# Kernel optimization log

Hardware: AMD Instinct MI355X
Metric: run time of the kernel (lower is better)

Reference implementation:

```python
import jax, jax.numpy as jnp
import numpy as np

B, S, E, H = 2, 2048, 1024, 16
Dh = E // H  # 64
KEEP = 0.9   # 1 - dropout_p
INV_SCALE = 1.0  # forward() default; call site does not pass inv_scale


def setup_inputs() -> dict:
    key = jax.random.key(0)
    ks = jax.random.split(key, 12)
    query = jax.random.normal(ks[0], (B, S, E), dtype=jnp.float32)
    key_t = jax.random.normal(ks[1], (B, S, E), dtype=jnp.float32)
    value = jax.random.normal(ks[2], (B, S, E), dtype=jnp.float32)
    attn_mask = jax.random.randint(ks[3], (B, S), 0, 2, dtype=jnp.int32)
    # pre-scaled inverted dropout keep-mask (deterministic stand-in for F.dropout)
    dropout_mask = (jax.random.uniform(ks[4], (B, H, S, S)) < KEEP).astype(jnp.float32) / KEEP
    Wq = jax.random.normal(ks[5], (E, E), dtype=jnp.float32) * 0.02
    bq = jnp.zeros((E,), dtype=jnp.float32)
    Wk = jax.random.normal(ks[6], (E, E), dtype=jnp.float32) * 0.02
    bk = jnp.zeros((E,), dtype=jnp.float32)
    Wv = jax.random.normal(ks[7], (E, E), dtype=jnp.float32) * 0.02
    bv = jnp.zeros((E,), dtype=jnp.float32)
    return {"query": query, "key": key_t, "value": value, "attn_mask": attn_mask,
            "dropout_mask": dropout_mask, "Wq": Wq, "bq": bq, "Wk": Wk, "bk": bk,
            "Wv": Wv, "bv": bv}


def _heads(x, W, b):
    # Linear then split heads: (B,S,E) -> (B,H,S,Dh)
    y = x @ W.T + b
    return y.reshape(B, S, H, Dh).transpose(0, 2, 1, 3)


def reference(query, key, value, attn_mask, dropout_mask, Wq, bq, Wk, bk, Wv, bv):
    q = _heads(query, Wq, bq)
    k = _heads(key, Wk, bk)
    v = _heads(value, Wv, bv)
    scores = jnp.einsum("bhqd,bhkd->bhqk", q, k) / INV_SCALE
    pad = (attn_mask == 0)[:, None, None, :]  # (B,1,1,S) True = masked
    scores = jnp.where(pad, -jnp.inf, scores)
    attn = jax.nn.softmax(scores, axis=-1) * dropout_mask
    out = jnp.einsum("bhqk,bhkd->bhqd", attn, v)  # (B,H,S,Dh)
    return out
```

## Files before the change

kernel.cpp:

```cpp
#include <hip/hip_runtime.h>

#define B_ 2
#define S_ 2048
#define E_ 1024
#define H_ 16
#define DH 64
#define MM (B_*S_)
#define BHN (B_*H_)
#define KSPLIT 4

typedef unsigned short u16;
typedef unsigned int u32;
typedef __attribute__((ext_vector_type(8))) __bf16 bf16x8;
typedef __attribute__((ext_vector_type(8))) _Float16 f16x8;
typedef __attribute__((ext_vector_type(4))) float f32x4;
typedef __attribute__((ext_vector_type(8))) u16 u16x8;
typedef __attribute__((ext_vector_type(4))) u16 u16x4;

static __device__ __forceinline__ u16 f2bf(float f) {
  u32 u = __builtin_bit_cast(u32, f);
  u += 0x7fffu + ((u >> 16) & 1u);
  return (u16)(u >> 16);
}
static __device__ __forceinline__ float bf2f(u16 h) {
  return __builtin_bit_cast(float, (u32)h << 16);
}
static __device__ __forceinline__ u32 sw(u32 byte) {
  return byte ^ (((byte >> 7) & 7u) << 4);
}
static __device__ __forceinline__ bf16x8 frag(const u16* lds, u32 byte) {
  return *(const bf16x8*)((const char*)lds + byte);
}
static __device__ __forceinline__ f16x8 frag16(const u16* lds, u32 byte) {
  return *(const f16x8*)((const char*)lds + byte);
}
static __device__ __forceinline__ f32x4 mfma_bf(bf16x8 a, bf16x8 b, f32x4 c) {
  return __builtin_amdgcn_mfma_f32_16x16x32_bf16(a, b, c, 0, 0, 0);
}
static __device__ __forceinline__ f32x4 mfma_f16(f16x8 a, f16x8 b, f32x4 c) {
  return __builtin_amdgcn_mfma_f32_16x16x32_f16(a, b, c, 0, 0, 0);
}
static __device__ __forceinline__ void gload_lds16(const u16* g, u16* lds_base) {
  __builtin_amdgcn_global_load_lds(
      (const __attribute__((address_space(1))) u32*)g,
      (__attribute__((address_space(3))) u32*)lds_base, 16, 0, 0);
}

#define L2E 1.44269504088896340736f

struct SplitArg { const float* s; u16* h; u16* l; int n4; };

__global__ void split6_kernel(SplitArg a0, SplitArg a1, SplitArg a2,
                              SplitArg a3, SplitArg a4, SplitArg a5) {
  SplitArg A = (blockIdx.z == 0) ? a0 : (blockIdx.z == 1) ? a1 : (blockIdx.z == 2) ? a2
             : (blockIdx.z == 3) ? a3 : (blockIdx.z == 4) ? a4 : a5;
  int i = blockIdx.x * blockDim.x + threadIdx.x;
  int stride = gridDim.x * blockDim.x;
  if (A.l) {
    for (; i < A.n4; i += stride) {
      float4 v = ((const float4*)A.s)[i];
      u16x4 h, l;
      h.x = f2bf(v.x); l.x = f2bf(v.x - bf2f(h.x));
      h.y = f2bf(v.y); l.y = f2bf(v.y - bf2f(h.y));
      h.z = f2bf(v.z); l.z = f2bf(v.z - bf2f(h.z));
      h.w = f2bf(v.w); l.w = f2bf(v.w - bf2f(h.w));
      ((u16x4*)A.h)[i] = h;
      ((u16x4*)A.l)[i] = l;
    }
  } else {
    for (; i < A.n4; i += stride) {
      float4 v = ((const float4*)A.s)[i];
      u16x4 h;
      h.x = f2bf(v.x); h.y = f2bf(v.y); h.z = f2bf(v.z); h.w = f2bf(v.w);
      ((u16x4*)A.h)[i] = h;
    }
  }
}

__global__ void pack_mask(const int* __restrict__ am, u32* __restrict__ pm) {
  int w = threadIdx.x;
  if (w < 128) {
    int base = (w >> 6) * 2048 + (w & 63) * 32;
    u32 bits = 0;
#pragma unroll
    for (int j = 0; j < 8; ++j) {
      int4 v = *(const int4*)(am + base + j * 4);
      bits |= (v.x ? 1u : 0u) << (4 * j) | (v.y ? 1u : 0u) << (4 * j + 1) |
              (v.z ? 1u : 0u) << (4 * j + 2) | (v.w ? 1u : 0u) << (4 * j + 3);
    }
    pm[w] = bits;
  }
}

struct ProjArgs {
  const u16* xhi; const u16* xlo; const u16* whi; const u16* wlo;
  const float* bias; u16* ohi; int mode;
};

__global__ __launch_bounds__(256, 3) void proj_gemm(ProjArgs a0, ProjArgs a1, ProjArgs a2) {
  ProjArgs A = (blockIdx.z == 0) ? a0 : (blockIdx.z == 1) ? a1 : a2;
  __shared__ u16 As[128 * 64];
  __shared__ u16 Bs[128 * 64];
  const int t = threadIdx.x;
  const int l = t & 63, wid = t >> 6;
  const int g = l >> 4, ln = l & 15;
  const int wm = wid >> 1, wn = wid & 1;
  int bid = blockIdx.y * 8 + blockIdx.x;
  int sid = (bid & 7) * 32 + (bid >> 3);
  const int m0 = (sid >> 3) * 128, e0 = (sid & 7) * 128;

  f32x4 acc[4][4] = {};
  const int nkt = (A.mode == 2) ? 32 : 48;

  for (int kt = 0; kt < nkt; ++kt) {
    int kp = kt * 64;
    const u16* asrc = (kp < 2048) ? A.xhi : A.xlo;
    const u16* bsrc = (kp < 1024 || kp >= 2048) ? A.whi : A.wlo;
    int kc = kp & 1023;
#pragma unroll
    for (int r = 0; r < 4; ++r) {
      int cr = wid * 4 + r;
      int row = cr * 8 + (l >> 3);
      int col = (l & 7) * 8;
      gload_lds16(asrc + (size_t)(m0 + row) * 1024 + kc + col, As + cr * 512);
      gload_lds16(bsrc + (size_t)(e0 + row) * 1024 + kc + col, Bs + cr * 512);
    }
    __syncthreads();
#pragma unroll
    for (int ks = 0; ks < 2; ++ks) {
      bf16x8 af[4], bfv[4];
#pragma unroll
      for (int i = 0; i < 4; ++i) {
        af[i] = frag(As, (u32)(wm * 64 + i * 16 + ln) * 128 + ks * 64 + g * 16);
        bfv[i] = frag(Bs, (u32)(wn * 64 + i * 16 + ln) * 128 + ks * 64 + g * 16);
      }
#pragma unroll
      for (int i = 0; i < 4; ++i)
#pragma unroll
        for (int j = 0; j < 4; ++j)
          acc[i][j] = mfma_bf(af[i], bfv[j], acc[i][j]);
    }
    __syncthreads();
  }

#pragma unroll
  for (int i = 0; i < 4; ++i) {
#pragma unroll
    for (int j = 0; j < 4; ++j) {
      int e = e0 + wn * 64 + j * 16 + ln;
      int h = e >> 6, d = e & 63;
      float bias = A.bias[e];
      if (A.mode < 2) {
#pragma unroll
        for (int r = 0; r < 4; ++r) {
          int m = m0 + wm * 64 + i * 16 + g * 4 + r;
          float v = acc[i][j][r] + bias;
          if (A.mode == 0) v *= L2E;
          int b = m >> 11, s = m & 2047;
          size_t idx = ((size_t)((b * 16 + h) * 2048 + s)) * 64 + d;
          A.ohi[idx] = __builtin_bit_cast(u16, (_Float16)v);
        }
      } else {
        int m = m0 + wm * 64 + i * 16 + g * 4;
        int b = m >> 11, s = m & 2047;
        u16x4 pv;
#pragma unroll
        for (int r = 0; r < 4; ++r)
          pv[r] = __builtin_bit_cast(u16, (__bf16)(acc[i][j][r] + bias));
        size_t idx = ((size_t)((b * 16 + h) * 64 + d)) * 2048 + s;
        *(u16x4*)(A.ohi + idx) = pv;
      }
    }
  }
}

__global__ __launch_bounds__(256, 3) void attn_kernel(
    const u16* __restrict__ qf, const u16* __restrict__ kf,
    const u16* __restrict__ vt, const u32* __restrict__ pm,
    const float* __restrict__ dmask, float* __restrict__ opart,
    float* __restrict__ zpart) {
  __shared__ u16 Ks[2][64 * 64];
  __shared__ u16 Vs[2][64 * 64];
  __shared__ u16 Ps[4 * 16 * 64];

  const int t = threadIdx.x, l = t & 63, wid = t >> 6;
  const int g = l >> 4, ln = l & 15;

  int bid = blockIdx.y * 32 + blockIdx.x;
  int sid = (bid & 7) * 128 + (bid >> 3);
  const int qt = sid & 31, bh = sid >> 5, b = bh >> 4;
  const int kc = blockIdx.z;
  const int q0 = qt * 64;
  const int qrow = q0 + wid * 16 + ln;
  const size_t qg = ((size_t)bh * 2048 + qrow) * 64;
  const u32* pmb = pm + b * 64;

  f16x8 qv[2];
#pragma unroll
  for (int ks = 0; ks < 2; ++ks)
    qv[ks] = *(const f16x8*)(qf + qg + ks * 32 + g * 8);

  const float* dmp = dmask + ((size_t)bh * 2048 + qrow) * 2048 + 4 * g;
  const int c0 = wid * 64 + l, c1 = wid * 64 + 256 + l;
  const int s0 = c0 ^ ((c0 >> 3) & 7), s1 = c1 ^ ((c1 >> 3) & 7);
  const u16* kp0 = kf + (size_t)bh * 2048 * 64 + s0 * 8;
  const u16* kp1 = kf + (size_t)bh * 2048 * 64 + s1 * 8;
  const u16* vp0 = vt + ((size_t)bh * 64 + (s0 >> 3)) * 2048 + (s0 & 7) * 8;
  const u16* vp1 = vt + ((size_t)bh * 64 + (s1 >> 3)) * 2048 + (s1 & 7) * 8;

  auto stage_tile = [&](int buf, int kt2) {
    u16* kd = Ks[buf];
    u16* vd = Vs[buf];
    gload_lds16(kp0 + (size_t)kt2 * 4096, kd + (wid * 64) * 8);
    gload_lds16(kp1 + (size_t)kt2 * 4096, kd + (wid * 64 + 256) * 8);
    gload_lds16(vp0 + kt2 * 64, vd + (wid * 64) * 8);
    gload_lds16(vp1 + kt2 * 64, vd + (wid * 64 + 256) * 8);
  };

  const int kt2_0 = kc * 8, kt2_last = kc * 8 + 7;

  stage_tile(0, kt2_0);
  float4 dmc[4], dmn[4];
#pragma unroll
  for (int i = 0; i < 4; ++i)
    dmc[i] = *(const float4*)(dmp + (size_t)kt2_0 * 64 + i * 16);

  f32x4 O[4] = {};
  float Zacc = 0.f;
  const u32 psbase = (u32)(wid * 2048 + ln * 128);
  u32 pw[4], pr[2];
#pragma unroll
  for (int i = 0; i < 4; ++i) pw[i] = sw(psbase + i * 32 + g * 8);
#pragma unroll
  for (int ks = 0; ks < 2; ++ks) pr[ks] = sw(psbase + ks * 64 + g * 16);

  for (int kt = 0; kt < 8; ++kt) {
    const int buf = kt & 1;
    const int kt2 = kc * 8 + kt;
    const int ktn = (kt < 7) ? kt2 + 1 : kt2_last;

    __builtin_amdgcn_s_barrier();
    __builtin_amdgcn_sched_barrier(0);

    stage_tile(buf ^ 1, ktn);
#pragma unroll
    for (int i = 0; i < 4; ++i)
      dmn[i] = *(const float4*)(dmp + (size_t)ktn * 64 + i * 16);

    asm volatile("s_waitcnt vmcnt(8)" ::: "memory");
    __builtin_amdgcn_sched_barrier(0);
    __builtin_amdgcn_s_barrier();
    __builtin_amdgcn_sched_barrier(0);

    u32 m0 = pmb[2 * kt2], m1 = pmb[2 * kt2 + 1];

    f32x4 sc[4] = {};
#pragma unroll
    for (int ks = 0; ks < 2; ++ks) {
#pragma unroll
      for (int i = 0; i < 4; ++i) {
        f16x8 ak = frag16(Ks[buf], sw((u32)((i * 16 + ln) * 128 + ks * 64 + g * 16)));
        sc[i] = mfma_f16(ak, qv[ks], sc[i]);
      }
    }

#pragma unroll
    for (int i = 0; i < 4; ++i) {
      u32 mm = (i < 2 ? m0 : m1) >> (((i & 1) << 4) + 4 * g);
      float e0 = (mm & 1u) ? exp2f(sc[i][0]) : 0.f;
      float e1 = (mm & 2u) ? exp2f(sc[i][1]) : 0.f;
      float e2 = (mm & 4u) ? exp2f(sc[i][2]) : 0.f;
      float e3 = (mm & 8u) ? exp2f(sc[i][3]) : 0.f;
      Zacc += (e0 + e1) + (e2 + e3);
      u16x4 p;
      p.x = __builtin_bit_cast(u16, (__bf16)(e0 * dmc[i].x));
      p.y = __builtin_bit_cast(u16, (__bf16)(e1 * dmc[i].y));
      p.z = __builtin_bit_cast(u16, (__bf16)(e2 * dmc[i].z));
      p.w = __builtin_bit_cast(u16, (__bf16)(e3 * dmc[i].w));
      *(u16x4*)((char*)Ps + pw[i]) = p;
    }

#pragma unroll
    for (int ks = 0; ks < 2; ++ks) {
      bf16x8 bP = frag(Ps, pr[ks]);
#pragma unroll
      for (int id = 0; id < 4; ++id) {
        bf16x8 aV = frag(Vs[buf], sw((u32)((id * 16 + ln) * 128 + ks * 64 + g * 16)));
        O[id] = mfma_bf(aV, bP, O[id]);
      }
    }

#pragma unroll
    for (int i = 0; i < 4; ++i) dmc[i] = dmn[i];
  }

  float z = Zacc;
  z += __shfl_xor(z, 16, 64);
  z += __shfl_xor(z, 32, 64);
  const int row = bh * 2048 + qrow;
  if (g == 0) zpart[kc * (BHN * S_) + row] = z;

  float* opb = opart + ((size_t)kc * (BHN * S_) + row) * 64;
#pragma unroll
  for (int id = 0; id < 4; ++id) {
    float4 o;
    o.x = O[id][0]; o.y = O[id][1]; o.z = O[id][2]; o.w = O[id][3];
    *(float4*)(opb + id * 16 + 4 * g) = o;
  }
}

__global__ void combine_kernel(const float* __restrict__ op,
                               const float* __restrict__ zp,
                               float* __restrict__ out) {
  int tid = blockIdx.x * blockDim.x + threadIdx.x;
  int row = tid >> 4, d4 = tid & 15;
  float4 o = make_float4(0.f, 0.f, 0.f, 0.f);
  float z = 0.f;
#pragma unroll
  for (int kc = 0; kc < KSPLIT; ++kc) {
    float4 v = *(const float4*)(op + ((size_t)kc * (BHN * S_) + row) * 64 + d4 * 4);
    o.x += v.x; o.y += v.y; o.z += v.z; o.w += v.w;
    z += zp[kc * (BHN * S_) + row];
  }
  float rz = 1.f / z;
  float4 r;
  r.x = o.x * rz; r.y = o.y * rz; r.z = o.z * rz; r.w = o.w * rz;
  *(float4*)(out + (size_t)row * 64 + d4 * 4) = r;
}

extern "C" void kernel_launch(void* const* d_in, const int* in_sizes, int n_in,
                              void* d_out, int out_size, void* d_ws, size_t ws_size,
                              hipStream_t stream) {
  const float* query = (const float*)d_in[0];
  const float* keyt  = (const float*)d_in[1];
  const float* value = (const float*)d_in[2];
  const int*   amask = (const int*)d_in[3];
  const float* dmask = (const float*)d_in[4];
  const float* Wq = (const float*)d_in[5];
  const float* bq = (const float*)d_in[6];
  const float* Wk = (const float*)d_in[7];
  const float* bk = (const float*)d_in[8];
  const float* Wv = (const float*)d_in[9];
  const float* bv = (const float*)d_in[10];

  char* ws = (char*)d_ws;
  size_t off = 0;
  auto alloc = [&](size_t bytes) {
    char* p = ws + off;
    off += (bytes + 255) & ~(size_t)255;
    return p;
  };
  const size_t XB = (size_t)MM * E_ * sizeof(u16);
  const size_t WB = (size_t)E_ * E_ * sizeof(u16);

  u16 *xh[3], *xl[3], *wh[3], *wl[3];
  for (int i = 0; i < 3; ++i) { xh[i] = (u16*)alloc(XB); xl[i] = (u16*)alloc(XB); }
  for (int i = 0; i < 3; ++i) { wh[i] = (u16*)alloc(WB); wl[i] = (u16*)alloc(WB); }
  u16* q_f16 = (u16*)alloc(XB);
  u16* k_f16 = (u16*)alloc(XB);
  u16* v_t   = (u16*)alloc(XB);
  u32* pmask = (u32*)alloc(512);
  float* opart = (float*)alloc((size_t)KSPLIT * BHN * S_ * 64 * 4);
  float* zpart = (float*)alloc((size_t)KSPLIT * BHN * S_ * 4);
  if (off > ws_size) return;

  SplitArg sa[6] = {
      {query, xh[0], xl[0], MM * E_ / 4}, {keyt, xh[1], xl[1], MM * E_ / 4},
      {value, xh[2], nullptr, MM * E_ / 4}, {Wq, wh[0], wl[0], E_ * E_ / 4},
      {Wk, wh[1], wl[1], E_ * E_ / 4},    {Wv, wh[2], wl[2], E_ * E_ / 4},
  };
  split6_kernel<<<dim3(512, 1, 6), 256, 0, stream>>>(sa[0], sa[1], sa[2], sa[3], sa[4], sa[5]);
  pack_mask<<<1, 128, 0, stream>>>(amask, pmask);

  ProjArgs pa[3] = {
      {xh[0], xl[0], wh[0], wl[0], bq, q_f16, 0},
      {xh[1], xl[1], wh[1], wl[1], bk, k_f16, 1},
      {xh[2], nullptr, wh[2], wl[2], bv, v_t, 2},
  };
  proj_gemm<<<dim3(8, 32, 3), 256, 0, stream>>>(pa[0], pa[1], pa[2]);

  attn_kernel<<<dim3(32, 32, KSPLIT), 256, 0, stream>>>(
      q_f16, k_f16, v_t, pmask, dmask, opart, zpart);

  combine_kernel<<<(BHN * S_ * 64 / 4) / 256, 256, 0, stream>>>(
      opart, zpart, (float*)d_out);
}
```

Baseline: 286.3 us.

## Stage dropout mask tiles into LDS via async global_load_lds

The attention kernel now stages the 64x64 fp32 dropout-mask tile into a double-buffered, XOR-swizzled LDS buffer with global_load_lds, alongside K and V. Previously each thread issued strided float4 register loads for the mask. The intent is to coalesce the dominant mask traffic and fold it into the existing async prefetch pipeline. It adds 32 KB of LDS per block, so launch bounds drop from 3 to 2 blocks per CU. The vmcnt(8) wait was not updated, even though each stage now issues 8 loads instead of 4, which may change how much overlap remains.

```diff
diff --git a/kernel.cpp b/kernel.cpp
--- a/kernel.cpp
+++ b/kernel.cpp
@@ -40,7 +40,7 @@
 static __device__ __forceinline__ f32x4 mfma_f16(f16x8 a, f16x8 b, f32x4 c) {
   return __builtin_amdgcn_mfma_f32_16x16x32_f16(a, b, c, 0, 0, 0);
 }
-static __device__ __forceinline__ void gload_lds16(const u16* g, u16* lds_base) {
+static __device__ __forceinline__ void gload_lds16(const void* g, void* lds_base) {
   __builtin_amdgcn_global_load_lds(
       (const __attribute__((address_space(1))) u32*)g,
       (__attribute__((address_space(3))) u32*)lds_base, 16, 0, 0);
@@ -174,13 +174,14 @@
   }
 }
 
-__global__ __launch_bounds__(256, 3) void attn_kernel(
+__global__ __launch_bounds__(256, 2) void attn_kernel(
     const u16* __restrict__ qf, const u16* __restrict__ kf,
     const u16* __restrict__ vt, const u32* __restrict__ pm,
     const float* __restrict__ dmask, float* __restrict__ opart,
     float* __restrict__ zpart) {
   __shared__ u16 Ks[2][64 * 64];
   __shared__ u16 Vs[2][64 * 64];
+  __shared__ float Dm[2][64 * 64];
   __shared__ u16 Ps[4 * 16 * 64];
 
   const int t = threadIdx.x, l = t & 63, wid = t >> 6;
@@ -200,7 +201,6 @@
   for (int ks = 0; ks < 2; ++ks)
     qv[ks] = *(const f16x8*)(qf + qg + ks * 32 + g * 8);
 
-  const float* dmp = dmask + ((size_t)bh * 2048 + qrow) * 2048 + 4 * g;
   const int c0 = wid * 64 + l, c1 = wid * 64 + 256 + l;
   const int s0 = c0 ^ ((c0 >> 3) & 7), s1 = c1 ^ ((c1 >> 3) & 7);
   const u16* kp0 = kf + (size_t)bh * 2048 * 64 + s0 * 8;
@@ -208,31 +208,42 @@
   const u16* vp0 = vt + ((size_t)bh * 64 + (s0 >> 3)) * 2048 + (s0 & 7) * 8;
   const u16* vp1 = vt + ((size_t)bh * 64 + (s1 >> 3)) * 2048 + (s1 & 7) * 8;
 
+  const float* dmbase = dmask + ((size_t)bh * 2048 + q0) * 2048;
+  int dmrowq[4]; int dmcolq[4];
+#pragma unroll
+  for (int r = 0; r < 4; ++r) {
+    int c = r * 256 + t;
+    dmrowq[r] = c >> 4;
+    dmcolq[r] = ((c & 15) ^ ((c >> 4) & 7)) * 4;
+  }
+
   auto stage_tile = [&](int buf, int kt2) {
-    u16* kd = Ks[buf];
-    u16* vd = Vs[buf];
-    gload_lds16(kp0 + (size_t)kt2 * 4096, kd + (wid * 64) * 8);
-    gload_lds16(kp1 + (size_t)kt2 * 4096, kd + (wid * 64 + 256) * 8);
-    gload_lds16(vp0 + kt2 * 64, vd + (wid * 64) * 8);
-    gload_lds16(vp1 + kt2 * 64, vd + (wid * 64 + 256) * 8);
+    gload_lds16(kp0 + (size_t)kt2 * 4096, Ks[buf] + (wid * 64) * 8);
+    gload_lds16(kp1 + (size_t)kt2 * 4096, Ks[buf] + (wid * 64 + 256) * 8);
+    gload_lds16(vp0 + kt2 * 64, Vs[buf] + (wid * 64) * 8);
+    gload_lds16(vp1 + kt2 * 64, Vs[buf] + (wid * 64 + 256) * 8);
+    const float* dsrc = dmbase + kt2 * 64;
+#pragma unroll
+    for (int r = 0; r < 4; ++r)
+      gload_lds16(dsrc + (size_t)dmrowq[r] * 2048 + dmcolq[r],
+                  Dm[buf] + (r * 256 + t) * 4);
   };
 
-  const int kt2_0 = kc * 8, kt2_last = kc * 8 + 7;
-
-  stage_tile(0, kt2_0);
-  float4 dmc[4], dmn[4];
-#pragma unroll
-  for (int i = 0; i < 4; ++i)
-    dmc[i] = *(const float4*)(dmp + (size_t)kt2_0 * 64 + i * 16);
+  const int kt2_last = kc * 8 + 7;
+
+  stage_tile(0, kc * 8);
 
   f32x4 O[4] = {};
   float Zacc = 0.f;
   const u32 psbase = (u32)(wid * 2048 + ln * 128);
-  u32 pw[4], pr[2];
+  u32 pw[4], pr[2], dmoff[4];
 #pragma unroll
   for (int i = 0; i < 4; ++i) pw[i] = sw(psbase + i * 32 + g * 8);
 #pragma unroll
   for (int ks = 0; ks < 2; ++ks) pr[ks] = sw(psbase + ks * 64 + g * 16);
+#pragma unroll
+  for (int i = 0; i < 4; ++i)
+    dmoff[i] = (u32)(((wid * 16 + ln) * 256 + i * 64 + g * 16) ^ ((ln & 7) << 4));
 
   for (int kt = 0; kt < 8; ++kt) {
     const int buf = kt & 1;
@@ -243,9 +254,6 @@
     __builtin_amdgcn_sched_barrier(0);
 
     stage_tile(buf ^ 1, ktn);
-#pragma unroll
-    for (int i = 0; i < 4; ++i)
-      dmn[i] = *(const float4*)(dmp + (size_t)ktn * 64 + i * 16);
 
     asm volatile("s_waitcnt vmcnt(8)" ::: "memory");
     __builtin_amdgcn_sched_barrier(0);
@@ -266,6 +274,7 @@
 
 #pragma unroll
     for (int i = 0; i < 4; ++i) {
+      f32x4 dm = *(const f32x4*)((const char*)Dm[buf] + dmoff[i]);
       u32 mm = (i < 2 ? m0 : m1) >> (((i & 1) << 4) + 4 * g);
       float e0 = (mm & 1u) ? exp2f(sc[i][0]) : 0.f;
       float e1 = (mm & 2u) ? exp2f(sc[i][1]) : 0.f;
@@ -273,10 +282,10 @@
       float e3 = (mm & 8u) ? exp2f(sc[i][3]) : 0.f;
       Zacc += (e0 + e1) + (e2 + e3);
       u16x4 p;
-      p.x = __builtin_bit_cast(u16, (__bf16)(e0 * dmc[i].x));
-      p.y = __builtin_bit_cast(u16, (__bf16)(e1 * dmc[i].y));
-      p.z = __builtin_bit_cast(u16, (__bf16)(e2 * dmc[i].z));
-      p.w = __builtin_bit_cast(u16, (__bf16)(e3 * dmc[i].w));
+      p.x = __builtin_bit_cast(u16, (__bf16)(e0 * dm[0]));
+      p.y = __builtin_bit_cast(u16, (__bf16)(e1 * dm[1]));
+      p.z = __builtin_bit_cast(u16, (__bf16)(e2 * dm[2]));
+      p.w = __builtin_bit_cast(u16, (__bf16)(e3 * dm[3]));
       *(u16x4*)((char*)Ps + pw[i]) = p;
     }
 
@@ -289,9 +298,6 @@
         O[id] = mfma_bf(aV, bP, O[id]);
       }
     }
-
-#pragma unroll
-    for (int i = 0; i < 4; ++i) dmc[i] = dmn[i];
   }
 
   float z = Zacc;
```

Measured after the change: 289.2 us. About the same (+1.0%).
